# Kernel optimization log

Measured on AMD Instinct MI355X. Metric: run time of the kernel, lower is better.

## Reference

```python
import jax, jax.numpy as jnp
import numpy as np

N_EVENTS = 131072
N_FEATURES = 128
N_GLOBAL = 64
HIDDEN = 512
N_BRANCHES = 2


def setup_inputs() -> dict:
    key = jax.random.key(0)
    ks = jax.random.split(key, 4)
    x = jax.random.normal(ks[0], (N_EVENTS, N_FEATURES), dtype=jnp.float32)
    global_features = jax.random.normal(ks[1], (N_EVENTS, N_GLOBAL), dtype=jnp.float32)
    # proj_nn params: Linear(192->512) + LeakyReLU + Linear(512->256)
    W1 = jax.random.normal(ks[2], (N_FEATURES + N_GLOBAL, HIDDEN), dtype=jnp.float32) / np.sqrt(N_FEATURES + N_GLOBAL)
    b1 = jnp.zeros((HIDDEN,), dtype=jnp.float32)
    W2 = jax.random.normal(ks[3], (HIDDEN, N_BRANCHES * N_FEATURES), dtype=jnp.float32) / np.sqrt(HIDDEN)
    b2 = jnp.zeros((N_BRANCHES * N_FEATURES,), dtype=jnp.float32)
    # isplit=0: root node idxs = arange(n_events)
    parents_idxs = jnp.arange(N_EVENTS, dtype=jnp.int64 if jax.config.jax_enable_x64 else jnp.int32)
    return {"x": x, "global_features": global_features, "W1": W1, "b1": b1,
            "W2": W2, "b2": b2, "parents_idxs": parents_idxs}


def reference(x, global_features, W1, b1, W2, b2, parents_idxs):
    n_events, n_features = x.shape
    n_branches = N_BRANCHES
    n_parents = parents_idxs.shape[0] // n_events  # = 1 at isplit=0
    # gather parent node features and per-event global features
    parent_global = global_features[parents_idxs % n_events, :]   # [P*E, G]
    parents_ftxs = x[parents_idxs, :]                             # [P*E, F]
    # proj_nn: Linear -> LeakyReLU -> Linear
    h = jnp.concatenate([parents_ftxs, parent_global], axis=1)
    h = jax.nn.leaky_relu(h @ W1 + b1)                            # slope 0.01, torch default
    proj_ftx = h @ W2 + b2                                        # [P*E, B*F]
    # reshape_features: out[p, b, e] = proj[e + p*E, b*F:(b+1)*F]
    children_ftxs = (proj_ftx
                     .reshape(n_parents, n_events, n_branches, n_features)
                     .transpose(0, 2, 1, 3)
                     .reshape(n_parents * n_branches * n_events, n_features))
    return jnp.concatenate([x, children_ftxs], axis=0)
```

## Files before the change

kernel.cpp:

```cpp
#include <hip/hip_runtime.h>
#include <hip/hip_bf16.h>

#define NEV 131072
#define NF 128
#define NG 64
#define KIN 192
#define NH 512
#define NOUT 256
#define BM 128
#define NT 512
#define NBLK (NEV / BM)
#define LDS128 131072

typedef __bf16 bf16x8 __attribute__((ext_vector_type(8)));
typedef __bf16 bf16x4 __attribute__((ext_vector_type(4)));
typedef float f32x4 __attribute__((ext_vector_type(4)));

__device__ __forceinline__ int a_off(int r, int cb) { return r * 384 + (cb ^ ((r & 7) << 4)); }
__device__ __forceinline__ int h_off(int r, int cb) { return r * 1024 + (cb ^ ((r & 7) << 4)); }

__global__ void pack_w(const float* __restrict__ W1, const float* __restrict__ W2,
                       __bf16* __restrict__ w1p, __bf16* __restrict__ w2p) {
    int t = blockIdx.x * blockDim.x + threadIdx.x;
    if (t < KIN * NH) {
        int j = t & 7;
        int lane = (t >> 3) & 63;
        int n = (t >> 9) & 3;
        int r = t >> 11;
        int kk = r % 6;
        int wc = r / 6;
        int lg = lane >> 4, lr = lane & 15;
        int k = kk * 32 + lg * 8 + j;
        int col = wc * 64 + n * 16 + lr;
        w1p[t] = (__bf16)W1[(size_t)k * NH + col];
    } else {
        int u = t - KIN * NH;
        if (u < NH * NOUT) {
            int j = u & 7;
            int lane = (u >> 3) & 63;
            int n = (u >> 9) & 1;
            int r = u >> 10;
            int kk = r & 15;
            int wc = r >> 4;
            int lg = lane >> 4, lr = lane & 15;
            int k = kk * 32 + lg * 8 + j;
            int col = wc * 32 + n * 16 + lr;
            w2p[u] = (__bf16)W2[(size_t)k * NOUT + col];
        }
    }
}

__global__ __launch_bounds__(NT)
__attribute__((amdgpu_waves_per_eu(2, 2))) void fused128(
        const float* __restrict__ x, const float* __restrict__ gf,
        const __bf16* __restrict__ w1p, const float* __restrict__ b1,
        const __bf16* __restrict__ w2p, const float* __restrict__ b2,
        const int* __restrict__ idx, float* __restrict__ out) {
    extern __shared__ __align__(16) unsigned char smem[];

    const int tid = threadIdx.x;
    const int wc = tid >> 6;
    const int lane = tid & 63;
    const int lg = lane >> 4;
    const int lr = lane & 15;
    const int row0 = blockIdx.x * BM;

    bf16x8 bq0[4], bq1[4];
    {
        const __bf16* wp = w1p;
        asm volatile("" : "+s"(wp));
#pragma unroll
        for (int n = 0; n < 4; ++n)
            bq0[n] = *(const bf16x8*)(wp + (size_t)((wc * 6 + 0) * 4 + n) * 512 + lane * 8);
#pragma unroll
        for (int n = 0; n < 4; ++n)
            bq1[n] = *(const bf16x8*)(wp + (size_t)((wc * 6 + 1) * 4 + n) * 512 + lane * 8);
    }

    const f32x4* x4 = (const f32x4*)x;
    const f32x4* g4 = (const f32x4*)gf;
    f32x4* o4 = (f32x4*)out;
#pragma unroll
    for (int q = tid; q < BM * (NF / 4); q += NT) {
        int r = q >> 5, c4 = q & 31;
        int e = row0 + r;
        int p = idx[e];
        f32x4 v = x4[(size_t)e * 32 + c4];
        __builtin_nontemporal_store(v, &o4[(size_t)e * 32 + c4]);
        f32x4 vs = v;
        if (p != e) vs = x4[(size_t)p * 32 + c4];
        bf16x4 tb = {(__bf16)vs[0], (__bf16)vs[1], (__bf16)vs[2], (__bf16)vs[3]};
        *(bf16x4*)(smem + a_off(r, c4 * 8)) = tb;
    }
#pragma unroll
    for (int q = tid; q < BM * (NG / 4); q += NT) {
        int r = q >> 4, c4 = q & 15;
        int e = row0 + r;
        int p = idx[e] & (NEV - 1);
        f32x4 vs = g4[(size_t)p * 16 + c4];
        bf16x4 tb = {(__bf16)vs[0], (__bf16)vs[1], (__bf16)vs[2], (__bf16)vs[3]};
        *(bf16x4*)(smem + a_off(r, 256 + c4 * 8)) = tb;
    }
    __syncthreads();

    f32x4 acc1T[4][8] = {};
#pragma unroll
    for (int kk = 0; kk < KIN / 32; ++kk) {
        bf16x8 bq2[4];
        if (kk + 2 < KIN / 32) {
            const __bf16* wp = w1p;
            asm volatile("" : "+s"(wp));
#pragma unroll
            for (int n = 0; n < 4; ++n)
                bq2[n] = *(const bf16x8*)(wp + (size_t)((wc * 6 + kk + 2) * 4 + n) * 512 + lane * 8);
        }
        int kbyte = kk * 64 + lg * 16;
        bf16x8 a[8];
#pragma unroll
        for (int m = 0; m < 8; ++m)
            a[m] = *(const bf16x8*)(smem + a_off(m * 16 + lr, kbyte));
        __builtin_amdgcn_s_setprio(1);
#pragma unroll
        for (int n = 0; n < 4; ++n)
#pragma unroll
            for (int m = 0; m < 8; ++m)
                acc1T[n][m] = __builtin_amdgcn_mfma_f32_16x16x32_bf16(bq0[n], a[m], acc1T[n][m], 0, 0, 0);
        __builtin_amdgcn_s_setprio(0);
#pragma unroll
        for (int n = 0; n < 4; ++n) { bq0[n] = bq1[n]; bq1[n] = bq2[n]; }
        __builtin_amdgcn_sched_barrier(0);
    }

    bf16x8 cq0[2], cq1[2];
    {
        const __bf16* wp = w2p;
        asm volatile("" : "+s"(wp));
#pragma unroll
        for (int n = 0; n < 2; ++n)
            cq0[n] = *(const bf16x8*)(wp + (size_t)((wc * 16 + 0) * 2 + n) * 512 + lane * 8);
#pragma unroll
        for (int n = 0; n < 2; ++n)
            cq1[n] = *(const bf16x8*)(wp + (size_t)((wc * 16 + 1) * 2 + n) * 512 + lane * 8);
    }
    __syncthreads();

#pragma unroll
    for (int n = 0; n < 4; ++n) {
        int c0 = wc * 64 + n * 16 + lg * 4;
        f32x4 bb = *(const f32x4*)(b1 + c0);
#pragma unroll
        for (int m = 0; m < 8; ++m) {
            int e = m * 16 + lr;
            bf16x4 tb;
#pragma unroll
            for (int i = 0; i < 4; ++i) {
                float v = acc1T[n][m][i] + bb[i];
                v = (v >= 0.f) ? v : 0.01f * v;
                tb[i] = (__bf16)v;
            }
            *(bf16x4*)(smem + h_off(e, c0 * 2)) = tb;
        }
    }
    __syncthreads();

    f32x4 acc2T[2][8] = {};
#pragma unroll
    for (int kk = 0; kk < NH / 32; ++kk) {
        bf16x8 cq2[2];
        if (kk + 2 < NH / 32) {
            const __bf16* wp = w2p;
            asm volatile("" : "+s"(wp));
#pragma unroll
            for (int n = 0; n < 2; ++n)
                cq2[n] = *(const bf16x8*)(wp + (size_t)((wc * 16 + kk + 2) * 2 + n) * 512 + lane * 8);
        }
        int kbyte = kk * 64 + lg * 16;
        bf16x8 a2[8];
#pragma unroll
        for (int m = 0; m < 8; ++m)
            a2[m] = *(const bf16x8*)(smem + h_off(m * 16 + lr, kbyte));
        __builtin_amdgcn_s_setprio(1);
#pragma unroll
        for (int n = 0; n < 2; ++n)
#pragma unroll
            for (int m = 0; m < 8; ++m)
                acc2T[n][m] = __builtin_amdgcn_mfma_f32_16x16x32_bf16(cq0[n], a2[m], acc2T[n][m], 0, 0, 0);
        __builtin_amdgcn_s_setprio(0);
#pragma unroll
        for (int n = 0; n < 2; ++n) { cq0[n] = cq1[n]; cq1[n] = cq2[n]; }
        __builtin_amdgcn_sched_barrier(0);
    }

    float* ob = out + ((size_t)NEV * (1 + (wc >> 2))) * NF;
#pragma unroll
    for (int m = 0; m < 8; ++m) {
        size_t ebase = (size_t)(row0 + m * 16 + lr) * NF;
#pragma unroll
        for (int n = 0; n < 2; ++n) {
            int col = wc * 32 + n * 16 + lg * 4;
            f32x4 bb = *(const f32x4*)(b2 + col);
            f32x4 v = acc2T[n][m] + bb;
            __builtin_nontemporal_store(v, (f32x4*)(ob + ebase + (col & 127)));
        }
    }
}

template <bool TW>
__global__ __launch_bounds__(512, 2) void fused_mlp(
        const float* __restrict__ x, const float* __restrict__ gf,
        const __bf16* __restrict__ w1p, const float* __restrict__ W1f,
        const float* __restrict__ b1,
        const __bf16* __restrict__ w2p, const float* __restrict__ W2f,
        const float* __restrict__ b2,
        const int* __restrict__ idx,
        float* __restrict__ out) {
    __shared__ __align__(16) unsigned char smem[65536];

    const int tid = threadIdx.x;
    const int wid = tid >> 6;
    const int lane = tid & 63;
    const int lg = lane >> 4;
    const int lr = lane & 15;
    const int row0 = blockIdx.x * 64;

    bf16x8 b1r[KIN / 32][4];
#pragma unroll
    for (int kk = 0; kk < KIN / 32; ++kk)
#pragma unroll
        for (int n = 0; n < 4; ++n) {
            if (TW) {
                b1r[kk][n] = *(const bf16x8*)(w1p + (size_t)(((wid * 6 + kk) * 4 + n) * 64 + lane) * 8);
            } else {
                int col = wid * 64 + n * 16 + lr;
                const float* wcp = W1f + (size_t)(kk * 32 + lg * 8) * NH + col;
#pragma unroll
                for (int i = 0; i < 8; ++i) b1r[kk][n][i] = (__bf16)wcp[(size_t)i * NH];
            }
        }

    const f32x4* x4 = (const f32x4*)x;
    const f32x4* g4 = (const f32x4*)gf;
    f32x4* o4 = (f32x4*)out;
    for (int q = tid; q < 64 * (NF / 4); q += 512) {
        int r = q >> 5, c4 = q & 31;
        int e = row0 + r;
        int p = idx[e];
        f32x4 v = x4[(size_t)e * 32 + c4];
        __builtin_nontemporal_store(v, &o4[(size_t)e * 32 + c4]);
        f32x4 vs = v;
        if (p != e) vs = x4[(size_t)p * 32 + c4];
        bf16x4 tb = {(__bf16)vs[0], (__bf16)vs[1], (__bf16)vs[2], (__bf16)vs[3]};
        *(bf16x4*)(smem + a_off(r, c4 * 8)) = tb;
    }
    for (int q = tid; q < 64 * (NG / 4); q += 512) {
        int r = q >> 4, c4 = q & 15;
        int e = row0 + r;
        int p = idx[e] & (NEV - 1);
        f32x4 vs = g4[(size_t)p * 16 + c4];
        bf16x4 tb = {(__bf16)vs[0], (__bf16)vs[1], (__bf16)vs[2], (__bf16)vs[3]};
        *(bf16x4*)(smem + a_off(r, 256 + c4 * 8)) = tb;
    }
    __syncthreads();

    f32x4 acc1T[4][4] = {};
#pragma unroll
    for (int kk = 0; kk < KIN / 32; ++kk) {
        int kbyte = kk * 64 + lg * 16;
        bf16x8 a[4];
#pragma unroll
        for (int m = 0; m < 4; ++m)
            a[m] = *(const bf16x8*)(smem + a_off(m * 16 + lr, kbyte));
        __builtin_amdgcn_s_setprio(1);
#pragma unroll
        for (int n = 0; n < 4; ++n)
#pragma unroll
            for (int m = 0; m < 4; ++m)
                acc1T[n][m] = __builtin_amdgcn_mfma_f32_16x16x32_bf16(b1r[kk][n], a[m], acc1T[n][m], 0, 0, 0);
        __builtin_amdgcn_s_setprio(0);
    }

    bf16x8 b2r[NH / 32][2];
#pragma unroll
    for (int kk = 0; kk < NH / 32; ++kk)
#pragma unroll
        for (int n = 0; n < 2; ++n) {
            if (TW) {
                b2r[kk][n] = *(const bf16x8*)(w2p + (size_t)(((wid * 16 + kk) * 2 + n) * 64 + lane) * 8);
            } else {
                int col = wid * 32 + n * 16 + lr;
                const float* wcp = W2f + (size_t)(kk * 32 + lg * 8) * NOUT + col;
#pragma unroll
                for (int i = 0; i < 8; ++i) b2r[kk][n][i] = (__bf16)wcp[(size_t)i * NOUT];
            }
        }

    __syncthreads();

#pragma unroll
    for (int n = 0; n < 4; ++n) {
        f32x4 bb = *(const f32x4*)(b1 + wid * 64 + n * 16 + lg * 4);
        int cb = (wid * 64 + n * 16 + lg * 4) * 2;
#pragma unroll
        for (int m = 0; m < 4; ++m) {
            int e = m * 16 + lr;
            bf16x4 tb;
#pragma unroll
            for (int i = 0; i < 4; ++i) {
                float v = acc1T[n][m][i] + bb[i];
                v = (v >= 0.f) ? v : 0.01f * v;
                tb[i] = (__bf16)v;
            }
            *(bf16x4*)(smem + h_off(e, cb)) = tb;
        }
    }
    __syncthreads();

    f32x4 acc2T[2][4] = {};
#pragma unroll
    for (int kk = 0; kk < NH / 32; ++kk) {
        int kbyte = kk * 64 + lg * 16;
        bf16x8 a2[4];
#pragma unroll
        for (int m = 0; m < 4; ++m)
            a2[m] = *(const bf16x8*)(smem + h_off(m * 16 + lr, kbyte));
        __builtin_amdgcn_s_setprio(1);
#pragma unroll
        for (int n = 0; n < 2; ++n)
#pragma unroll
            for (int m = 0; m < 4; ++m)
                acc2T[n][m] = __builtin_amdgcn_mfma_f32_16x16x32_bf16(b2r[kk][n], a2[m], acc2T[n][m], 0, 0, 0);
        __builtin_amdgcn_s_setprio(0);
    }

    float* ob = out + ((size_t)NEV * (1 + (wid >> 2))) * NF;
#pragma unroll
    for (int m = 0; m < 4; ++m) {
        size_t ebase = (size_t)(row0 + m * 16 + lr) * NF;
#pragma unroll
        for (int n = 0; n < 2; ++n) {
            int col = wid * 32 + n * 16 + lg * 4;
            f32x4 bb = *(const f32x4*)(b2 + col);
            f32x4 v = acc2T[n][m] + bb;
            __builtin_nontemporal_store(v, (f32x4*)(ob + ebase + (col & 127)));
        }
    }
}

extern "C" void kernel_launch(void* const* d_in, const int* in_sizes, int n_in,
                              void* d_out, int out_size, void* d_ws, size_t ws_size,
                              hipStream_t stream) {
    const float* x  = (const float*)d_in[0];
    const float* gf = (const float*)d_in[1];
    const float* W1 = (const float*)d_in[2];
    const float* b1 = (const float*)d_in[3];
    const float* W2 = (const float*)d_in[4];
    const float* b2 = (const float*)d_in[5];
    const int*  idx = (const int*)d_in[6];
    float* out = (float*)d_out;

    const size_t wbytes = (size_t)(KIN * NH + NH * NOUT) * sizeof(__bf16);
    int tot = KIN * NH + NH * NOUT;

    if (ws_size >= wbytes) {
        __bf16* w1p = (__bf16*)d_ws;
        __bf16* w2p = w1p + KIN * NH;
        pack_w<<<(tot + 511) / 512, 512, 0, stream>>>(W1, W2, w1p, w2p);
        hipError_t st = hipFuncSetAttribute(
            (const void*)fused128, hipFuncAttributeMaxDynamicSharedMemorySize, LDS128);
        if (st == hipSuccess) {
            fused128<<<NBLK, NT, LDS128, stream>>>(x, gf, w1p, b1, w2p, b2, idx, out);
        } else {
            fused_mlp<true><<<NEV / 64, 512, 0, stream>>>(x, gf, w1p, nullptr, b1,
                                                          w2p, nullptr, b2, idx, out);
        }
    } else {
        fused_mlp<false><<<NEV / 64, 512, 0, stream>>>(x, gf, nullptr, W1, b1,
                                                       nullptr, W2, b2, idx, out);
    }
}
```

Baseline: 100.8 us.

## Make fused MLP kernel loop over four row tiles with next-tile input prefetch

Each block now processes four consecutive 128-row tiles instead of one, cutting the grid from 1024 to 256 blocks. While the current tile's GEMMs run, the next tile's x and global-feature rows are loaded into registers and written to LDS after the second GEMM. This overlaps input loads with compute and amortises per-block setup. The cost is more register pressure, extra barriers, and less parallelism: 256 blocks is roughly one per CU on a 256-CU device, so load imbalance or latency exposure may grow.

```diff
diff --git a/kernel.cpp b/kernel.cpp
--- a/kernel.cpp
+++ b/kernel.cpp
@@ -9,7 +9,8 @@
 #define NOUT 256
 #define BM 128
 #define NT 512
-#define NBLK (NEV / BM)
+#define TILES 4
+#define NPERS (NEV / (BM * TILES))
 #define LDS128 131072
 
 typedef __bf16 bf16x8 __attribute__((ext_vector_type(8)));
@@ -51,7 +52,7 @@
 }
 
 __global__ __launch_bounds__(NT)
-__attribute__((amdgpu_waves_per_eu(2, 2))) void fused128(
+__attribute__((amdgpu_waves_per_eu(2, 2))) void fused_pers(
         const float* __restrict__ x, const float* __restrict__ gf,
         const __bf16* __restrict__ w1p, const float* __restrict__ b1,
         const __bf16* __restrict__ w2p, const float* __restrict__ b2,
@@ -63,7 +64,14 @@
     const int lane = tid & 63;
     const int lg = lane >> 4;
     const int lr = lane & 15;
-    const int row0 = blockIdx.x * BM;
+
+    const f32x4* x4 = (const f32x4*)x;
+    const f32x4* g4 = (const f32x4*)gf;
+    f32x4* o4 = (f32x4*)out;
+    const int xr = tid >> 5, xc = tid & 31;
+    const int gr = tid >> 4, gc = tid & 15;
+
+    int row0 = blockIdx.x * (BM * TILES);
 
     bf16x8 bq0[4], bq1[4];
     {
@@ -76,10 +84,6 @@
         for (int n = 0; n < 4; ++n)
             bq1[n] = *(const bf16x8*)(wp + (size_t)((wc * 6 + 1) * 4 + n) * 512 + lane * 8);
     }
-
-    const f32x4* x4 = (const f32x4*)x;
-    const f32x4* g4 = (const f32x4*)gf;
-    f32x4* o4 = (f32x4*)out;
 #pragma unroll
     for (int q = tid; q < BM * (NF / 4); q += NT) {
         int r = q >> 5, c4 = q & 31;
@@ -103,105 +107,159 @@
     }
     __syncthreads();
 
-    f32x4 acc1T[4][8] = {};
-#pragma unroll
-    for (int kk = 0; kk < KIN / 32; ++kk) {
-        bf16x8 bq2[4];
-        if (kk + 2 < KIN / 32) {
+    f32x4 xv[8], gv[4];
+
+    for (int t = 0; t < TILES; ++t) {
+        f32x4 acc1T[4][8] = {};
+#pragma unroll
+        for (int kk = 0; kk < KIN / 32; ++kk) {
+            bf16x8 bq2[4];
+            if (kk + 2 < KIN / 32) {
+                const __bf16* wp = w1p;
+                asm volatile("" : "+s"(wp));
+#pragma unroll
+                for (int n = 0; n < 4; ++n)
+                    bq2[n] = *(const bf16x8*)(wp + (size_t)((wc * 6 + kk + 2) * 4 + n) * 512 + lane * 8);
+            }
+            int kbyte = kk * 64 + lg * 16;
+            bf16x8 a[8];
+#pragma unroll
+            for (int m = 0; m < 8; ++m)
+                a[m] = *(const bf16x8*)(smem + a_off(m * 16 + lr, kbyte));
+            __builtin_amdgcn_s_setprio(1);
+#pragma unroll
+            for (int n = 0; n < 4; ++n)
+#pragma unroll
+                for (int m = 0; m < 8; ++m)
+                    acc1T[n][m] = __builtin_amdgcn_mfma_f32_16x16x32_bf16(bq0[n], a[m], acc1T[n][m], 0, 0, 0);
+            __builtin_amdgcn_s_setprio(0);
+#pragma unroll
+            for (int n = 0; n < 4; ++n) { bq0[n] = bq1[n]; bq1[n] = bq2[n]; }
+            __builtin_amdgcn_sched_barrier(0);
+        }
+        __syncthreads();
+
+        if (t + 1 < TILES) {
+            int nrow = row0 + BM;
+#pragma unroll
+            for (int s = 0; s < 8; ++s) {
+                int e = nrow + xr + 16 * s;
+                xv[s] = x4[(size_t)e * 32 + xc];
+            }
+#pragma unroll
+            for (int s = 0; s < 4; ++s) {
+                int e = nrow + gr + 32 * s;
+                int p = idx[e] & (NEV - 1);
+                gv[s] = g4[(size_t)p * 16 + gc];
+            }
+        }
+
+#pragma unroll
+        for (int n = 0; n < 4; ++n) {
+            int c0 = wc * 64 + n * 16 + lg * 4;
+            f32x4 bb = *(const f32x4*)(b1 + c0);
+#pragma unroll
+            for (int m = 0; m < 8; ++m) {
+                int e = m * 16 + lr;
+                bf16x4 tb;
+#pragma unroll
+                for (int i = 0; i < 4; ++i) {
+                    float v = acc1T[n][m][i] + bb[i];
+                    v = (v >= 0.f) ? v : 0.01f * v;
+                    tb[i] = (__bf16)v;
+                }
+                *(bf16x4*)(smem + h_off(e, c0 * 2)) = tb;
+            }
+        }
+
+        bf16x8 cq0[2], cq1[2];
+        {
+            const __bf16* wp = w2p;
+            asm volatile("" : "+s"(wp));
+#pragma unroll
+            for (int n = 0; n < 2; ++n)
+                cq0[n] = *(const bf16x8*)(wp + (size_t)((wc * 16 + 0) * 2 + n) * 512 + lane * 8);
+#pragma unroll
+            for (int n = 0; n < 2; ++n)
+                cq1[n] = *(const bf16x8*)(wp + (size_t)((wc * 16 + 1) * 2 + n) * 512 + lane * 8);
+        }
+        __syncthreads();
+
+        f32x4 acc2T[2][8] = {};
+#pragma unroll
+        for (int kk = 0; kk < NH / 32; ++kk) {
+            bf16x8 cq2[2];
+            if (kk + 2 < NH / 32) {
+                const __bf16* wp = w2p;
+                asm volatile("" : "+s"(wp));
+#pragma unroll
+                for (int n = 0; n < 2; ++n)
+                    cq2[n] = *(const bf16x8*)(wp + (size_t)((wc * 16 + kk + 2) * 2 + n) * 512 + lane * 8);
+            }
+            int kbyte = kk * 64 + lg * 16;
+            bf16x8 a2[8];
+#pragma unroll
+            for (int m = 0; m < 8; ++m)
+                a2[m] = *(const bf16x8*)(smem + h_off(m * 16 + lr, kbyte));
+            __builtin_amdgcn_s_setprio(1);
+#pragma unroll
+            for (int n = 0; n < 2; ++n)
+#pragma unroll
+                for (int m = 0; m < 8; ++m)
+                    acc2T[n][m] = __builtin_amdgcn_mfma_f32_16x16x32_bf16(cq0[n], a2[m], acc2T[n][m], 0, 0, 0);
+            __builtin_amdgcn_s_setprio(0);
+#pragma unroll
+            for (int n = 0; n < 2; ++n) { cq0[n] = cq1[n]; cq1[n] = cq2[n]; }
+            __builtin_amdgcn_sched_barrier(0);
+        }
+        __syncthreads();
+
+        if (t + 1 < TILES) {
+            int nrow = row0 + BM;
+#pragma unroll
+            for (int s = 0; s < 8; ++s) {
+                int r = xr + 16 * s;
+                int e = nrow + r;
+                __builtin_nontemporal_store(xv[s], &o4[(size_t)e * 32 + xc]);
+                int p = idx[e];
+                f32x4 vs = xv[s];
+                if (p != e) vs = x4[(size_t)p * 32 + xc];
+                bf16x4 tb = {(__bf16)vs[0], (__bf16)vs[1], (__bf16)vs[2], (__bf16)vs[3]};
+                *(bf16x4*)(smem + a_off(r, xc * 8)) = tb;
+            }
+#pragma unroll
+            for (int s = 0; s < 4; ++s) {
+                int r = gr + 32 * s;
+                bf16x4 tb = {(__bf16)gv[s][0], (__bf16)gv[s][1], (__bf16)gv[s][2], (__bf16)gv[s][3]};
+                *(bf16x4*)(smem + a_off(r, 256 + gc * 8)) = tb;
+            }
+        }
+
+        float* ob = out + ((size_t)NEV * (1 + (wc >> 2))) * NF;
+#pragma unroll
+        for (int m = 0; m < 8; ++m) {
+            size_t ebase = (size_t)(row0 + m * 16 + lr) * NF;
+#pragma unroll
+            for (int n = 0; n < 2; ++n) {
+                int col = wc * 32 + n * 16 + lg * 4;
+                f32x4 bb = *(const f32x4*)(b2 + col);
+                f32x4 v = acc2T[n][m] + bb;
+                __builtin_nontemporal_store(v, (f32x4*)(ob + ebase + (col & 127)));
+            }
+        }
+
+        if (t + 1 < TILES) {
             const __bf16* wp = w1p;
             asm volatile("" : "+s"(wp));
 #pragma unroll
             for (int n = 0; n < 4; ++n)
-                bq2[n] = *(const bf16x8*)(wp + (size_t)((wc * 6 + kk + 2) * 4 + n) * 512 + lane * 8);
-        }
-        int kbyte = kk * 64 + lg * 16;
-        bf16x8 a[8];
-#pragma unroll
-        for (int m = 0; m < 8; ++m)
-            a[m] = *(const bf16x8*)(smem + a_off(m * 16 + lr, kbyte));
-        __builtin_amdgcn_s_setprio(1);
-#pragma unroll
-        for (int n = 0; n < 4; ++n)
-#pragma unroll
-            for (int m = 0; m < 8; ++m)
-                acc1T[n][m] = __builtin_amdgcn_mfma_f32_16x16x32_bf16(bq0[n], a[m], acc1T[n][m], 0, 0, 0);
-        __builtin_amdgcn_s_setprio(0);
-#pragma unroll
-        for (int n = 0; n < 4; ++n) { bq0[n] = bq1[n]; bq1[n] = bq2[n]; }
-        __builtin_amdgcn_sched_barrier(0);
-    }
-
-    bf16x8 cq0[2], cq1[2];
-    {
-        const __bf16* wp = w2p;
-        asm volatile("" : "+s"(wp));
-#pragma unroll
-        for (int n = 0; n < 2; ++n)
-            cq0[n] = *(const bf16x8*)(wp + (size_t)((wc * 16 + 0) * 2 + n) * 512 + lane * 8);
-#pragma unroll
-        for (int n = 0; n < 2; ++n)
-            cq1[n] = *(const bf16x8*)(wp + (size_t)((wc * 16 + 1) * 2 + n) * 512 + lane * 8);
-    }
-    __syncthreads();
-
-#pragma unroll
-    for (int n = 0; n < 4; ++n) {
-        int c0 = wc * 64 + n * 16 + lg * 4;
-        f32x4 bb = *(const f32x4*)(b1 + c0);
-#pragma unroll
-        for (int m = 0; m < 8; ++m) {
-            int e = m * 16 + lr;
-            bf16x4 tb;
-#pragma unroll
-            for (int i = 0; i < 4; ++i) {
-                float v = acc1T[n][m][i] + bb[i];
-                v = (v >= 0.f) ? v : 0.01f * v;
-                tb[i] = (__bf16)v;
-            }
-            *(bf16x4*)(smem + h_off(e, c0 * 2)) = tb;
-        }
-    }
-    __syncthreads();
-
-    f32x4 acc2T[2][8] = {};
-#pragma unroll
-    for (int kk = 0; kk < NH / 32; ++kk) {
-        bf16x8 cq2[2];
-        if (kk + 2 < NH / 32) {
-            const __bf16* wp = w2p;
-            asm volatile("" : "+s"(wp));
-#pragma unroll
-            for (int n = 0; n < 2; ++n)
-                cq2[n] = *(const bf16x8*)(wp + (size_t)((wc * 16 + kk + 2) * 2 + n) * 512 + lane * 8);
-        }
-        int kbyte = kk * 64 + lg * 16;
-        bf16x8 a2[8];
-#pragma unroll
-        for (int m = 0; m < 8; ++m)
-            a2[m] = *(const bf16x8*)(smem + h_off(m * 16 + lr, kbyte));
-        __builtin_amdgcn_s_setprio(1);
-#pragma unroll
-        for (int n = 0; n < 2; ++n)
-#pragma unroll
-            for (int m = 0; m < 8; ++m)
-                acc2T[n][m] = __builtin_amdgcn_mfma_f32_16x16x32_bf16(cq0[n], a2[m], acc2T[n][m], 0, 0, 0);
-        __builtin_amdgcn_s_setprio(0);
-#pragma unroll
-        for (int n = 0; n < 2; ++n) { cq0[n] = cq1[n]; cq1[n] = cq2[n]; }
-        __builtin_amdgcn_sched_barrier(0);
-    }
-
-    float* ob = out + ((size_t)NEV * (1 + (wc >> 2))) * NF;
-#pragma unroll
-    for (int m = 0; m < 8; ++m) {
-        size_t ebase = (size_t)(row0 + m * 16 + lr) * NF;
-#pragma unroll
-        for (int n = 0; n < 2; ++n) {
-            int col = wc * 32 + n * 16 + lg * 4;
-            f32x4 bb = *(const f32x4*)(b2 + col);
-            f32x4 v = acc2T[n][m] + bb;
-            __builtin_nontemporal_store(v, (f32x4*)(ob + ebase + (col & 127)));
-        }
+                bq0[n] = *(const bf16x8*)(wp + (size_t)((wc * 6 + 0) * 4 + n) * 512 + lane * 8);
+#pragma unroll
+            for (int n = 0; n < 4; ++n)
+                bq1[n] = *(const bf16x8*)(wp + (size_t)((wc * 6 + 1) * 4 + n) * 512 + lane * 8);
+            __syncthreads();
+        }
+        row0 += BM;
     }
 }
 
@@ -366,9 +424,9 @@
         __bf16* w2p = w1p + KIN * NH;
         pack_w<<<(tot + 511) / 512, 512, 0, stream>>>(W1, W2, w1p, w2p);
         hipError_t st = hipFuncSetAttribute(
-            (const void*)fused128, hipFuncAttributeMaxDynamicSharedMemorySize, LDS128);
+            (const void*)fused_pers, hipFuncAttributeMaxDynamicSharedMemorySize, LDS128);
         if (st == hipSuccess) {
-            fused128<<<NBLK, NT, LDS128, stream>>>(x, gf, w1p, b1, w2p, b2, idx, out);
+            fused_pers<<<NPERS, NT, LDS128, stream>>>(x, gf, w1p, b1, w2p, b2, idx, out);
         } else {
             fused_mlp<true><<<NEV / 64, 512, 0, stream>>>(x, gf, w1p, nullptr, b1,
                                                           w2p, nullptr, b2, idx, out);
```

Measured after the change: 149.1 us. 1.48x slower.
